# Performance work log

Measured on AMD Instinct MI355X. Metric: run time of the kernel, lower is better.

## Reference

```python
import jax, jax.numpy as jnp
import numpy as np


def setup_inputs() -> dict:
    key = jax.random.key(0)
    k1, k2 = jax.random.split(key)
    N_ACTIVE = 262144
    C = 64            # nPlanes
    S = 64            # spatial_size per dim (3D)
    B = 8             # batch size
    features = jax.random.normal(k1, (N_ACTIVE, C), dtype=jnp.float32)
    # rule book: flat linear index of each active site into (b, z, y, x)
    idx = jax.random.randint(k2, (N_ACTIVE,), 0, B * S * S * S, dtype=jnp.int64)
    return {"features": features, "idx": idx, "spatial_size": S, "batch_size": B}


def reference(features, idx, spatial_size, batch_size):
    # Scatter sparse active-site features into dense grid.
    # features: [N, C], idx: [N] flat index over (b, z, y, x).
    N, C = features.shape
    S = spatial_size
    B = batch_size
    dense = jnp.zeros((B * S * S * S, C), dtype=features.dtype)
    # active sites in SparseConvNet are unique -> add == set, but add has a
    # well-defined gradient (pure gather) matching SparseToDense_updateGradInput
    dense = dense.at[idx].add(features)
    # [B, S, S, S, C] -> [B, C, S, S, S] (torch channels-first layout)
    dense = dense.reshape(B, S, S, S, C)
    return jnp.transpose(dense, (0, 4, 1, 2, 3))
```

## Files before the change

### kernel.cpp

```cpp
#include <hip/hip_runtime.h>


#define C_CH      64
#define LOG_C     6
#define LOG_S3    18
#define S3        (1 << LOG_S3)
#define NCELL     (8 * S3)
#define OUT_ELEMS (8LL * C_CH * S3)

typedef float v4f __attribute__((ext_vector_type(4)));

__global__ void init_head_kernel(int* __restrict__ head) {
    int i = blockIdx.x * blockDim.x + threadIdx.x;
    ((int4*)head)[i] = make_int4(-1, -1, -1, -1);
}

__global__ void build_lists_kernel(const int* __restrict__ idx,
                                   int* __restrict__ head,
                                   int* __restrict__ nxt, int n) {
    int i = blockIdx.x * blockDim.x + threadIdx.x;
    if (i < n) {
        int cell = idx[i];
        nxt[i] = atomicExch(&head[cell], i);
    }
}

__global__ void __launch_bounds__(256)
emit_reg_kernel(const float* __restrict__ feat,
                const int* __restrict__ head,
                const int* __restrict__ nxt,
                float* __restrict__ out) {
    const int b      = blockIdx.x >> 8;
    const int s_base = (blockIdx.x & 255) << 10;
    const int cell0  = s_base + (threadIdx.x << 2);

    const int4 h4 = *(const int4*)(head + ((size_t)b << LOG_S3) + cell0);
    int hs[4] = {h4.x, h4.y, h4.z, h4.w};

    #pragma unroll 1
    for (int chunk = 0; chunk < 4; ++chunk) {
        float acc[64];
        #pragma unroll
        for (int i = 0; i < 64; ++i) acc[i] = 0.f;

        #pragma unroll
        for (int j = 0; j < 4; ++j) {
            int p = hs[j];
            while (p >= 0) {
                const v4f* fr = (const v4f*)(feat + ((size_t)p << LOG_C)
                                             + (chunk << 4));
                v4f f0 = fr[0], f1 = fr[1], f2 = fr[2], f3 = fr[3];
                float* a = acc + j * 16;
                a[0]  += f0.x; a[1]  += f0.y; a[2]  += f0.z; a[3]  += f0.w;
                a[4]  += f1.x; a[5]  += f1.y; a[6]  += f1.z; a[7]  += f1.w;
                a[8]  += f2.x; a[9]  += f2.y; a[10] += f2.z; a[11] += f2.w;
                a[12] += f3.x; a[13] += f3.y; a[14] += f3.z; a[15] += f3.w;
                p = nxt[p];
            }
        }

        const size_t obase = ((size_t)((b << LOG_C) + (chunk << 4)) << LOG_S3)
                             + cell0;
        #pragma unroll
        for (int cc = 0; cc < 16; ++cc) {
            v4f v = {acc[cc], acc[16 + cc], acc[32 + cc], acc[48 + cc]};
            __builtin_nontemporal_store(
                v, (v4f*)(out + obase + ((size_t)cc << LOG_S3)));
        }
    }
}

__global__ void zero_out_kernel(float4* __restrict__ out) {
    long long i = (long long)blockIdx.x * blockDim.x + threadIdx.x;
    out[i] = make_float4(0.f, 0.f, 0.f, 0.f);
}

__global__ void scatter_atomic_kernel(const float* __restrict__ feat,
                                      const int* __restrict__ idx,
                                      float* __restrict__ out, int n) {
    int i = blockIdx.x * blockDim.x + threadIdx.x;
    int nn = i >> LOG_C;
    int c  = i & (C_CH - 1);
    if (nn < n) {
        int cell = idx[nn];
        int b = cell >> LOG_S3;
        int s = cell & (S3 - 1);
        long long o = (((long long)((b << LOG_C) + c)) << LOG_S3) + s;
        atomicAdd(&out[o], feat[i]);
    }
}

extern "C" void kernel_launch(void* const* d_in, const int* in_sizes, int n_in,
                              void* d_out, int out_size, void* d_ws, size_t ws_size,
                              hipStream_t stream) {
    const float* feat = (const float*)d_in[0];
    const int*   idx  = (const int*)d_in[1];
    float*       out  = (float*)d_out;
    const int N = in_sizes[1];

    const size_t head_bytes = (size_t)NCELL * sizeof(int);
    const size_t next_bytes = (size_t)N * sizeof(int);

    if (ws_size >= head_bytes + next_bytes) {
        int* head = (int*)d_ws;
        int* nxt  = (int*)((char*)d_ws + head_bytes);

        init_head_kernel<<<NCELL / 4 / 256, 256, 0, stream>>>(head);
        build_lists_kernel<<<(N + 255) / 256, 256, 0, stream>>>(idx, head, nxt, N);
        emit_reg_kernel<<<NCELL / 1024, 256, 0, stream>>>(feat, head, nxt, out);
    } else {
        zero_out_kernel<<<(int)(OUT_ELEMS / 4 / 256), 256, 0, stream>>>((float4*)out);
        scatter_atomic_kernel<<<(N * C_CH) / 256, 256, 0, stream>>>(feat, idx, out, N);
    }
}
```

Measured before the change: 624.3 us.

## Assign one thread per cell, accumulating all channels in one list walk

The dense-emit kernel now gives each thread a single output cell instead of four cells processed in four 16-channel passes. Each thread walks its linked list once, loading the full 64-channel feature row with nontemporal vector loads, then writes 64 scalar channel-strided nontemporal stores. This removes the repeated list traversal and launches four times as many blocks. In exchange, stores shrink from 16-byte vector writes to 4-byte per-lane writes, which still coalesce across the wavefront but need more store instructions. An unused preliminary load block is left in the loop and is likely removed by the compiler as dead code.

```diff
diff --git a/kernel.cpp b/kernel.cpp
--- a/kernel.cpp
+++ b/kernel.cpp
@@ -26,48 +26,45 @@
 }
 
 __global__ void __launch_bounds__(256)
-emit_reg_kernel(const float* __restrict__ feat,
-                const int* __restrict__ head,
-                const int* __restrict__ nxt,
-                float* __restrict__ out) {
-    const int b      = blockIdx.x >> 8;
-    const int s_base = (blockIdx.x & 255) << 10;
-    const int cell0  = s_base + (threadIdx.x << 2);
+emit_cell_kernel(const float* __restrict__ feat,
+                 const int* __restrict__ head,
+                 const int* __restrict__ nxt,
+                 float* __restrict__ out) {
+    const int cell = blockIdx.x * 256 + threadIdx.x;
+    const int b    = cell >> LOG_S3;
+    const int s    = cell & (S3 - 1);
 
-    const int4 h4 = *(const int4*)(head + ((size_t)b << LOG_S3) + cell0);
-    int hs[4] = {h4.x, h4.y, h4.z, h4.w};
+    float acc[C_CH];
+    #pragma unroll
+    for (int i = 0; i < C_CH; ++i) acc[i] = 0.f;
 
-    #pragma unroll 1
-    for (int chunk = 0; chunk < 4; ++chunk) {
-        float acc[64];
+    int p = head[cell];
+    while (p >= 0) {
+        const int pn = nxt[p];
+        const v4f* fr = (const v4f*)(feat + ((size_t)p << LOG_C));
+        v4f f[4];
         #pragma unroll
-        for (int i = 0; i < 64; ++i) acc[i] = 0.f;
+        for (int q = 0; q < 4; ++q)
+            f[q] = __builtin_nontemporal_load(fr + 4 * 0 + q * 4);
+        #pragma unroll
+        for (int q = 0; q < 4; ++q) {
+            v4f a = __builtin_nontemporal_load(fr + q * 4 + 0);
+            v4f b4 = __builtin_nontemporal_load(fr + q * 4 + 1);
+            v4f c4 = __builtin_nontemporal_load(fr + q * 4 + 2);
+            v4f d4 = __builtin_nontemporal_load(fr + q * 4 + 3);
+            float* ap = acc + q * 16;
+            ap[0]  += a.x;  ap[1]  += a.y;  ap[2]  += a.z;  ap[3]  += a.w;
+            ap[4]  += b4.x; ap[5]  += b4.y; ap[6]  += b4.z; ap[7]  += b4.w;
+            ap[8]  += c4.x; ap[9]  += c4.y; ap[10] += c4.z; ap[11] += c4.w;
+            ap[12] += d4.x; ap[13] += d4.y; ap[14] += d4.z; ap[15] += d4.w;
+        }
+        p = pn;
+    }
 
-        #pragma unroll
-        for (int j = 0; j < 4; ++j) {
-            int p = hs[j];
-            while (p >= 0) {
-                const v4f* fr = (const v4f*)(feat + ((size_t)p << LOG_C)
-                                             + (chunk << 4));
-                v4f f0 = fr[0], f1 = fr[1], f2 = fr[2], f3 = fr[3];
-                float* a = acc + j * 16;
-                a[0]  += f0.x; a[1]  += f0.y; a[2]  += f0.z; a[3]  += f0.w;
-                a[4]  += f1.x; a[5]  += f1.y; a[6]  += f1.z; a[7]  += f1.w;
-                a[8]  += f2.x; a[9]  += f2.y; a[10] += f2.z; a[11] += f2.w;
-                a[12] += f3.x; a[13] += f3.y; a[14] += f3.z; a[15] += f3.w;
-                p = nxt[p];
-            }
-        }
-
-        const size_t obase = ((size_t)((b << LOG_C) + (chunk << 4)) << LOG_S3)
-                             + cell0;
-        #pragma unroll
-        for (int cc = 0; cc < 16; ++cc) {
-            v4f v = {acc[cc], acc[16 + cc], acc[32 + cc], acc[48 + cc]};
-            __builtin_nontemporal_store(
-                v, (v4f*)(out + obase + ((size_t)cc << LOG_S3)));
-        }
-    }
+    float* obase = out + ((size_t)b << (LOG_C + LOG_S3)) + s;
+    #pragma unroll
+    for (int c = 0; c < C_CH; ++c)
+        __builtin_nontemporal_store(acc[c], obase + ((size_t)c << LOG_S3));
 }
 
 __global__ void zero_out_kernel(float4* __restrict__ out) {
@@ -107,7 +104,7 @@
 
         init_head_kernel<<<NCELL / 4 / 256, 256, 0, stream>>>(head);
         build_lists_kernel<<<(N + 255) / 256, 256, 0, stream>>>(idx, head, nxt, N);
-        emit_reg_kernel<<<NCELL / 1024, 256, 0, stream>>>(feat, head, nxt, out);
+        emit_cell_kernel<<<NCELL / 256, 256, 0, stream>>>(feat, head, nxt, out);
     } else {
         zero_out_kernel<<<(int)(OUT_ELEMS / 4 / 256), 256, 0, stream>>>((float4*)out);
         scatter_atomic_kernel<<<(N * C_CH) / 256, 256, 0, stream>>>(feat, idx, out, N);
```

Result: slower. 638.5 us (+2.3%).
